# Performance work log

Hardware: AMD Instinct MI355X
Metric: run time of the kernel (lower is better)

Reference implementation:

```python
import jax, jax.numpy as jnp
import numpy as np
from jax import lax

V, E, H = 90000, 256, 512  # vocab, embed_dim, lstm_dim
B, TE, TD = 16, 64, 32     # batch, encoder time, decoder time
NEG = jnp.float32(-1e9)


def setup_inputs() -> dict:
    key = jax.random.key(0)
    ks = jax.random.split(key, 16)
    u = lambda k, shape, s: jax.random.uniform(k, shape, jnp.float32, -s, s)
    inp = {
        "encoder_inputs": jax.random.randint(ks[0], (B, TE), 0, V, dtype=jnp.int32),
        "decoder_inputs": jax.random.randint(ks[1], (B, TD), 0, V, dtype=jnp.int32),
        "encoder_lengths": jnp.maximum(jax.random.randint(ks[2], (B,), 1, TE + 1, dtype=jnp.int32), 1),
        "decoder_lengths": jnp.maximum(jax.random.randint(ks[3], (B,), 1, TD + 1, dtype=jnp.int32), 1),
        "embeddings": u(ks[4], (V, E), 1.0 / 16),
        # encoder BasicLSTMCell: kernel [E+H, 4H], bias [4H]
        "W_enc": u(ks[5], (E + H, 4 * H), 1.0 / np.sqrt(E + H)),
        "b_enc": jnp.zeros((4 * H,), jnp.float32),
        # decoder cell input = concat(embed, attention[H]) -> kernel [(E+H)+H, 4H]
        "W_dec": u(ks[6], (E + 2 * H, 4 * H), 1.0 / np.sqrt(E + 2 * H)),
        "b_dec": jnp.zeros((4 * H,), jnp.float32),
        # Bahdanau attention: memory layer, query layer, score vector v
        "W_mem": u(ks[7], (H, H), 1.0 / np.sqrt(H)),
        "W_query": u(ks[8], (H, H), 1.0 / np.sqrt(H)),
        "v_att": u(ks[9], (H,), 1.0 / np.sqrt(H)),
        # attention_layer: Dense(H, use_bias=False) on concat(cell_out, context)
        "W_attn": u(ks[10], (2 * H, H), 1.0 / np.sqrt(2 * H)),
        # output projection: Dense(90000, use_bias=False)
        "W_proj": u(ks[11], (H, V), 1.0 / np.sqrt(H)),
    }
    return inp


def _lstm_step(x, h, c, W, b):
    # TF BasicLSTMCell: gates i, j, f, o; forget_bias = 1.0
    z = jnp.concatenate([x, h], axis=-1) @ W + b
    i, j, f, o = jnp.split(z, 4, axis=-1)
    c2 = c * jax.nn.sigmoid(f + 1.0) + jax.nn.sigmoid(i) * jnp.tanh(j)
    h2 = jnp.tanh(c2) * jax.nn.sigmoid(o)
    return h2, c2


def reference(encoder_inputs, decoder_inputs, encoder_lengths, decoder_lengths,
              embeddings, W_enc, b_enc, W_dec, b_dec,
              W_mem, W_query, v_att, W_attn, W_proj):
    q_emb = embeddings[encoder_inputs]  # [B,TE,E]
    r_emb = embeddings[decoder_inputs]  # [B,TD,E]
    zeros_h = jnp.zeros((B, H), jnp.float32)

    # ---- encoder: dynamic_rnn semantics (zero outputs / frozen state past length)
    def enc_step(carry, xs):
        c, h = carry
        x_t, t = xs
        h2, c2 = _lstm_step(x_t, h, c, W_enc, b_enc)
        valid = (t < encoder_lengths)[:, None]
        h2 = jnp.where(valid, h2, h)
        c2 = jnp.where(valid, c2, c)
        return (c2, h2), jnp.where(valid, h2, 0.0)

    (c_e, h_e), enc_out = lax.scan(
        enc_step, (zeros_h, zeros_h),
        (q_emb.transpose(1, 0, 2), jnp.arange(TE)))
    enc_out = enc_out.transpose(1, 0, 2)  # [B,TE,H]

    keys = jnp.einsum('bth,hk->btk', enc_out, W_mem)  # memory layer
    enc_mask = jnp.arange(TE)[None, :] < encoder_lengths[:, None]  # [B,TE]

    # ---- decoder: AttentionWrapper(LSTM) + Bahdanau attention, per step
    def dec_step(carry, xs):
        c, h, attn = carry
        x_t, t = xs
        h2, c2 = _lstm_step(jnp.concatenate([x_t, attn], axis=-1), h, c, W_dec, b_dec)
        pq = h2 @ W_query  # [B,H]
        score = jnp.einsum('h,bth->bt', v_att, jnp.tanh(keys + pq[:, None, :]))
        score = jnp.where(enc_mask, score, NEG)
        align = jax.nn.softmax(score, axis=-1)
        ctx = jnp.einsum('bt,bth->bh', align, enc_out)
        attn2 = jnp.concatenate([h2, ctx], axis=-1) @ W_attn  # attention_layer
        logits_t = attn2 @ W_proj  # [B,V]
        # dynamic_decode zeros emissions once finished (t >= decoder_length)
        logits_t = jnp.where((t < decoder_lengths)[:, None], logits_t, 0.0)
        return (c2, h2, attn2), logits_t

    # initial state: zero_state cloned with cell_state = encoder final state
    _, logits = lax.scan(
        dec_step, (c_e, h_e, zeros_h),
        (r_emb.transpose(1, 0, 2), jnp.arange(TD)))
    return logits.transpose(1, 0, 2)  # [B,TD,V]
```

## Files before the change

kernel.cpp:

```cpp
#include <hip/hip_runtime.h>

#define E_  256
#define H_  512
#define B_  16
#define TE_ 64
#define TD_ 32
#define V_  90000
#define G4_ 2048
#define NBLK_ 128

typedef __attribute__((ext_vector_type(8))) short short8;
typedef __attribute__((ext_vector_type(4))) float f32x4;
typedef _Float16 half2_ __attribute__((ext_vector_type(2)));

__device__ __forceinline__ float sigm(float x) { return 1.f / (1.f + __expf(-x)); }
__device__ __forceinline__ float tanh_(float x) {
  float e = __expf(-2.f * fabsf(x));
  float r = (1.f - e) / (1.f + e);
  return x >= 0.f ? r : -r;
}
__device__ __forceinline__ unsigned short f2bf(float v) {
  union { float f; unsigned u; } c; c.f = v;
  unsigned r = c.u + 0x7FFFu + ((c.u >> 16) & 1u);
  return (unsigned short)(r >> 16);
}
__device__ __forceinline__ unsigned pack2(float a, float b) {
  union { unsigned u; _Float16 h[2]; } p;
  p.h[0] = (_Float16)a; p.h[1] = (_Float16)b;
  return p.u;
}
__device__ __forceinline__ float dot2u(unsigned w, unsigned h, float acc) {
#if __has_builtin(__builtin_amdgcn_fdot2)
  union { unsigned u; half2_ v; } a, b; a.u = w; b.u = h;
  return __builtin_amdgcn_fdot2(a.v, b.v, acc, false);
#else
  union { unsigned u; _Float16 h[2]; } a, b; a.u = w; b.u = h;
  return acc + (float)a.h[0] * (float)b.h[0] + (float)a.h[1] * (float)b.h[1];
#endif
}
__device__ __forceinline__ float dot8(uint4 w, uint4 h, float acc) {
  acc = dot2u(w.x, h.x, acc);
  acc = dot2u(w.y, h.y, acc);
  acc = dot2u(w.z, h.z, acc);
  acc = dot2u(w.w, h.w, acc);
  return acc;
}

__global__ __launch_bounds__(256) void k_cv(
    const float* __restrict__ W_enc, const float* __restrict__ W_dec,
    const float* __restrict__ W_query, const float* __restrict__ W_attn,
    const float* __restrict__ W_mem,
    uint4* __restrict__ Ue, uint4* __restrict__ Ud, uint4* __restrict__ Wq,
    uint4* __restrict__ Wa, uint4* __restrict__ Wm)
{
  int u = blockIdx.x * 256 + threadIdx.x;
  const float* src; uint4* dst; int C, r0, lu;
  if (u < 131072)      { src = W_enc;   dst = Ue; C = 2048; r0 = 256; lu = u; }
  else if (u < 393216) { src = W_dec;   dst = Ud; C = 2048; r0 = 256; lu = u - 131072; }
  else if (u < 425984) { src = W_query; dst = Wq; C = 512;  r0 = 0;   lu = u - 393216; }
  else if (u < 491520) { src = W_attn;  dst = Wa; C = 512;  r0 = 0;   lu = u - 425984; }
  else                 { src = W_mem;   dst = Wm; C = 512;  r0 = 0;   lu = u - 491520; }
  int kc = lu / C, col = lu - kc * C;
  union { uint4 v; _Float16 h[8]; } p;
  #pragma unroll
  for (int e = 0; e < 8; ++e)
    p.h[e] = (_Float16)src[(size_t)(r0 + kc * 8 + e) * C + col];
  dst[(size_t)kc * C + col] = p.v;
}

__global__ __launch_bounds__(256) void k_xg(
    const int* __restrict__ toks, const float* __restrict__ emb,
    const float* __restrict__ W, const float* __restrict__ bias,
    float* __restrict__ Xg)
{
  const int tid = threadIdx.x;
  const int cc = tid & 63;
  const int tg = tid >> 6;
  const int col = blockIdx.x * 64 + cc;
  const int t0 = blockIdx.y * 64 + tg * 16;
  const float* ep[16];
  #pragma unroll
  for (int i = 0; i < 16; ++i) ep[i] = emb + (size_t)toks[t0 + i] * E_;
  float acc[16];
  float bv = bias[col];
  #pragma unroll
  for (int i = 0; i < 16; ++i) acc[i] = bv;
  for (int k4 = 0; k4 < 64; ++k4) {
    float w0 = W[(size_t)(k4 * 4 + 0) * G4_ + col];
    float w1 = W[(size_t)(k4 * 4 + 1) * G4_ + col];
    float w2 = W[(size_t)(k4 * 4 + 2) * G4_ + col];
    float w3 = W[(size_t)(k4 * 4 + 3) * G4_ + col];
    #pragma unroll
    for (int i = 0; i < 16; ++i) {
      float4 e4 = *(const float4*)(ep[i] + k4 * 4);
      acc[i] += e4.x * w0 + e4.y * w1 + e4.z * w2 + e4.w * w3;
    }
  }
  #pragma unroll
  for (int i = 0; i < 16; ++i)
    Xg[(size_t)(t0 + i) * G4_ + col] = acc[i];
}

__device__ __forceinline__ void gbar(unsigned* bar, unsigned gen) {
  __syncthreads();
  if (threadIdx.x == 0) {
    __threadfence();
    __hip_atomic_fetch_add(bar, 1u, __ATOMIC_RELAXED, __HIP_MEMORY_SCOPE_AGENT);
    const unsigned tgt = gen * (unsigned)NBLK_;
    while (__hip_atomic_load(bar, __ATOMIC_RELAXED, __HIP_MEMORY_SCOPE_AGENT) < tgt)
      __builtin_amdgcn_s_sleep(1);
    __threadfence();
  }
  __syncthreads();
}

__global__ __launch_bounds__(512) void k_seq(
    const int* __restrict__ enc_len, const float* __restrict__ v_att,
    const float* __restrict__ Xge, const float* __restrict__ Xgd,
    const uint4* __restrict__ Ue, const uint4* __restrict__ Ud,
    const uint4* __restrict__ WqG, const uint4* __restrict__ WaG,
    const uint4* __restrict__ WmG,
    float* __restrict__ keys, unsigned* __restrict__ enc_f16,
    unsigned* __restrict__ hbuf, unsigned* __restrict__ abuf,
    unsigned short* __restrict__ attn_bf, unsigned* __restrict__ bar)
{
  __shared__ __align__(16) uint4 sU[128 * 16];
  __shared__ __align__(16) uint4 sE[64 * 16];
  __shared__ __align__(16) uint4 sI[128 * 16];
  __shared__ __align__(16) uint4 hbB[128];
  __shared__ float pacc[256];
  __shared__ float shx[4][16];
  __shared__ float shy[4][16];
  __shared__ float pqL[512];
  __shared__ float vlL[512];
  __shared__ float atf[512];
  __shared__ float scp[64][8];
  __shared__ float al64[64];
  __shared__ float ctp[256][2];

  const int tid = threadIdx.x, bid = blockIdx.x;
  const int tlo = tid & 255, hi = tid >> 8;
  const int b = tlo & 15, g = (tlo >> 4) & 3, hcl = tlo >> 6;
  const int wl = hcl * 4 + g;
  const int el = enc_len[b];
  const int elB = (bid < 16) ? enc_len[bid] : 0;
  unsigned gen = 0;

  for (int idx = tid; idx < 64 * 16; idx += 512) {
    int kc = idx >> 4, w = idx & 15;
    sE[idx] = Ue[(size_t)kc * 2048 + (w & 3) * 512 + bid * 4 + (w >> 2)];
  }
  for (int idx = tid; idx < 128 * 16; idx += 512) {
    int kc = idx >> 4, w = idx & 15;
    sU[idx] = Ud[(size_t)kc * 2048 + (w & 3) * 512 + bid * 4 + (w >> 2)];
  }
  if (tid < 32) abuf[bid * 32 + tid] = 0u;
  if (bid < 16) vlL[tid] = v_att[tid];

  float c = 0.f, hreg = 0.f;
  const uint4* hb4 = (const uint4*)hbuf;
  const uint4* ab4 = (const uint4*)abuf;
  const uint4* ef4 = (const uint4*)enc_f16;

  for (int t = 0; t < TE_; ++t) {
    for (int idx = tid; idx < 64 * 16; idx += 512) {
      int kc = idx >> 4, bb = idx & 15;
      uint4 v = {0u, 0u, 0u, 0u};
      if (t) v = hb4[bb * 64 + kc];
      sI[idx] = v;
    }
    __syncthreads();
    float acc;
    {
      const int kc0 = hi ? 32 : 0;
      acc = hi ? 0.f
               : Xge[(size_t)(b * TE_ + t) * G4_ + g * 512 + bid * 4 + hcl];
      const uint4* wp = sE + kc0 * 16 + wl;
      const uint4* ip = sI + kc0 * 16 + b;
      #pragma unroll 4
      for (int kc = 0; kc < 32; ++kc)
        acc = dot8(wp[kc * 16], ip[kc * 16], acc);
    }
    if (hi) pacc[tlo] = acc;
    __syncthreads();
    if (!hi) {
      acc += pacc[tlo];
      float v0 = acc;
      float v1 = __shfl_xor(v0, 16);
      float v2 = __shfl_xor(v0, 32);
      float v3 = __shfl_xor(v0, 48);
      float gi = (g == 0) ? v0 : (g == 1) ? v1 : (g == 2) ? v2 : v3;
      float gj = (g == 0) ? v1 : (g == 1) ? v0 : (g == 2) ? v3 : v2;
      float gf = (g == 0) ? v2 : (g == 1) ? v3 : (g == 2) ? v0 : v1;
      float go = (g == 0) ? v3 : (g == 1) ? v2 : (g == 2) ? v1 : v0;
      float c2 = c * sigm(gf + 1.f) + sigm(gi) * tanh_(gj);
      float h2 = tanh_(c2) * sigm(go);
      bool valid = t < el;
      c = valid ? c2 : c;
      hreg = valid ? h2 : hreg;
      if (g == 0) {
        shx[hcl][b] = hreg;
        shy[hcl][b] = valid ? h2 : 0.f;
      }
    }
    __syncthreads();
    if (tid < 32) {
      int bb = tid & 15, pr = tid >> 4;
      hbuf[bb * 256 + bid * 2 + pr] = pack2(shx[2 * pr][bb], shx[2 * pr + 1][bb]);
      enc_f16[(size_t)(bb * TE_ + t) * 256 + bid * 2 + pr] =
          pack2(shy[2 * pr][bb], shy[2 * pr + 1][bb]);
    }
    ++gen; gbar(bar, gen);
  }

  {
    for (int idx = tid; idx < 8 * 64; idx += 512) {
      int r = idx >> 6, kc = idx & 63;
      sI[idx] = ef4[(size_t)(bid * 8 + r) * 64 + kc];
    }
    __syncthreads();
    float a8[8] = {0.f, 0.f, 0.f, 0.f, 0.f, 0.f, 0.f, 0.f};
    const uint4* wm = WmG + tid;
    for (int kc = 0; kc < 64; ++kc) {
      uint4 w = wm[(size_t)kc * 512];
      #pragma unroll
      for (int r = 0; r < 8; ++r) a8[r] = dot8(w, sI[r * 64 + kc], a8[r]);
    }
    #pragma unroll
    for (int r = 0; r < 8; ++r)
      keys[(size_t)(bid * 8 + r) * 512 + tid] = a8[r];
    ++gen; gbar(bar, gen);
  }

  for (int t = 0; t < TD_; ++t) {
    for (int idx = tid; idx < 128 * 16; idx += 512) {
      int kc = idx >> 4, bb = idx & 15;
      sI[idx] = (kc < 64) ? ab4[bb * 64 + kc] : hb4[bb * 64 + (kc - 64)];
    }
    __syncthreads();
    float acc;
    {
      const int kc0 = hi ? 64 : 0;
      acc = hi ? 0.f
               : Xgd[(size_t)(b * TD_ + t) * G4_ + g * 512 + bid * 4 + hcl];
      const uint4* wp = sU + kc0 * 16 + wl;
      const uint4* ip = sI + kc0 * 16 + b;
      #pragma unroll 4
      for (int kc = 0; kc < 64; ++kc)
        acc = dot8(wp[kc * 16], ip[kc * 16], acc);
    }
    if (hi) pacc[tlo] = acc;
    __syncthreads();
    if (!hi) {
      acc += pacc[tlo];
      float v0 = acc;
      float v1 = __shfl_xor(v0, 16);
      float v2 = __shfl_xor(v0, 32);
      float v3 = __shfl_xor(v0, 48);
      float gi = (g == 0) ? v0 : (g == 1) ? v1 : (g == 2) ? v2 : v3;
      float gj = (g == 0) ? v1 : (g == 1) ? v0 : (g == 2) ? v3 : v2;
      float gf = (g == 0) ? v2 : (g == 1) ? v3 : (g == 2) ? v0 : v1;
      float go = (g == 0) ? v3 : (g == 1) ? v2 : (g == 2) ? v1 : v0;
      float c2 = c * sigm(gf + 1.f) + sigm(gi) * tanh_(gj);
      float h2 = tanh_(c2) * sigm(go);
      c = c2;
      if (g == 0) shx[hcl][b] = h2;
    }
    __syncthreads();
    if (tid < 32) {
      int bb = tid & 15, pr = tid >> 4;
      hbuf[bb * 256 + bid * 2 + pr] = pack2(shx[2 * pr][bb], shx[2 * pr + 1][bb]);
    }
    ++gen; gbar(bar, gen);

    if (bid < 16) {
      if (tid < 64) hbB[tid] = hb4[bid * 64 + tid];
      __syncthreads();
      {
        float a = 0.f;
        const uint4* wq = WqG + tid;
        #pragma unroll 4
        for (int kc = 0; kc < 64; ++kc)
          a = dot8(wq[(size_t)kc * 512], hbB[kc], a);
        pqL[tid] = a;
      }
      __syncthreads();
      {
        int tt = tid >> 3, q = tid & 7;
        const float4* kr = (const float4*)(keys + (size_t)(bid * TE_ + tt) * 512 + q * 64);
        const float4* pp = (const float4*)(pqL + q * 64);
        const float4* vp = (const float4*)(vlL + q * 64);
        float s = 0.f;
        #pragma unroll 4
        for (int i = 0; i < 16; ++i) {
          float4 k4 = kr[i], p4 = pp[i], v4 = vp[i];
          s += v4.x * tanh_(k4.x + p4.x) + v4.y * tanh_(k4.y + p4.y)
             + v4.z * tanh_(k4.z + p4.z) + v4.w * tanh_(k4.w + p4.w);
        }
        scp[tt][q] = s;
      }
      __syncthreads();
      if (tid < 64) {
        float sum = 0.f;
        #pragma unroll
        for (int q = 0; q < 8; ++q) sum += scp[tid][q];
        float sc = (tid < elB) ? sum : -1e9f;
        float m = sc;
        for (int o = 32; o > 0; o >>= 1) m = fmaxf(m, __shfl_xor(m, o));
        float p = __expf(sc - m);
        float l = p;
        for (int o = 32; o > 0; o >>= 1) l += __shfl_xor(l, o);
        al64[tid] = p / l;
      }
      __syncthreads();
      {
        const int j = tlo;
        float c0 = 0.f, c1 = 0.f;
        const unsigned* eb = enc_f16 + (size_t)(bid * TE_ + hi * 32) * 256 + j;
        #pragma unroll 8
        for (int t2 = 0; t2 < 32; ++t2) {
          union { unsigned u; _Float16 h[2]; } u2;
          u2.u = eb[(size_t)t2 * 256];
          float a = al64[hi * 32 + t2];
          c0 += a * (float)u2.h[0];
          c1 += a * (float)u2.h[1];
        }
        if (hi) { ctp[j][0] = c0; ctp[j][1] = c1; }
        __syncthreads();
        if (!hi)
          ((unsigned*)hbB)[256 + j] = pack2(c0 + ctp[j][0], c1 + ctp[j][1]);
        __syncthreads();
      }
      {
        float a = 0.f;
        const uint4* wa = WaG + tid;
        #pragma unroll 2
        for (int kc = 0; kc < 128; ++kc)
          a = dot8(wa[(size_t)kc * 512], hbB[kc], a);
        attn_bf[(size_t)(bid * TD_ + t) * 512 + tid] = f2bf(a);
        atf[tid] = a;
      }
      __syncthreads();
      if (tid < 256) abuf[bid * 256 + tid] = pack2(atf[2 * tid], atf[2 * tid + 1]);
    }
    ++gen; gbar(bar, gen);
  }
}

__global__ __launch_bounds__(512) void k_proj(
    const float* __restrict__ Wp, const unsigned short* __restrict__ Abf,
    const int* __restrict__ dec_len_g, float* __restrict__ out)
{
  __shared__ unsigned short Al[512 * 40];
  __shared__ unsigned short Bl[128 * 40];
  __shared__ int dl[16];
  const int tid = threadIdx.x;
  const int n0 = blockIdx.x * 128;
  const int wave = tid >> 6, lane = tid & 63;
  if (tid < 16) dl[tid] = dec_len_g[tid];
  f32x4 acc[4][8] = {};
  for (int kc = 0; kc < 16; ++kc) {
    const int k0 = kc * 32;
    {
      const unsigned short* src = Abf + (size_t)tid * 512 + k0;
      unsigned short* dst = Al + tid * 40;
      *(uint4*)(dst)      = *(const uint4*)(src);
      *(uint4*)(dst + 8)  = *(const uint4*)(src + 8);
      *(uint4*)(dst + 16) = *(const uint4*)(src + 16);
      *(uint4*)(dst + 24) = *(const uint4*)(src + 24);
    }
    {
      int kk = tid >> 4;
      int nn = (tid & 15) * 8;
      const float* src = Wp + (size_t)(k0 + kk) * V_ + n0 + nn;
      #pragma unroll
      for (int j = 0; j < 8; ++j) {
        float v = (n0 + nn + j < V_) ? src[j] : 0.f;
        Bl[(nn + j) * 40 + kk] = f2bf(v);
      }
    }
    __syncthreads();
    short8 bfr[8];
    #pragma unroll
    for (int nt = 0; nt < 8; ++nt)
      bfr[nt] = *(const short8*)&Bl[(nt * 16 + (lane & 15)) * 40 + (lane >> 4) * 8];
    #pragma unroll
    for (int mt = 0; mt < 4; ++mt) {
      short8 af = *(const short8*)&Al[(wave * 64 + mt * 16 + (lane & 15)) * 40 + (lane >> 4) * 8];
      #pragma unroll
      for (int nt = 0; nt < 8; ++nt)
        acc[mt][nt] = __builtin_amdgcn_mfma_f32_16x16x32_bf16(af, bfr[nt], acc[mt][nt], 0, 0, 0);
    }
    __syncthreads();
  }
  #pragma unroll
  for (int mt = 0; mt < 4; ++mt) {
    #pragma unroll
    for (int e = 0; e < 4; ++e) {
      int r = wave * 64 + mt * 16 + ((lane >> 4) << 2) + e;
      bool valid = (r & 31) < dl[r >> 5];
      #pragma unroll
      for (int nt = 0; nt < 8; ++nt) {
        int gcol = n0 + nt * 16 + (lane & 15);
        if (gcol < V_)
          out[(size_t)r * V_ + gcol] = valid ? acc[mt][nt][e] : 0.f;
      }
    }
  }
}

extern "C" void kernel_launch(void* const* d_in, const int* in_sizes, int n_in,
                              void* d_out, int out_size, void* d_ws, size_t ws_size,
                              hipStream_t stream) {
  const int* enc_in   = (const int*)d_in[0];
  const int* dec_in   = (const int*)d_in[1];
  const int* enc_len  = (const int*)d_in[2];
  const int* dec_len  = (const int*)d_in[3];
  const float* emb    = (const float*)d_in[4];
  const float* W_enc  = (const float*)d_in[5];
  const float* b_enc  = (const float*)d_in[6];
  const float* W_dec  = (const float*)d_in[7];
  const float* b_dec  = (const float*)d_in[8];
  const float* W_mem  = (const float*)d_in[9];
  const float* W_query= (const float*)d_in[10];
  const float* v_att  = (const float*)d_in[11];
  const float* W_attn = (const float*)d_in[12];
  const float* W_proj = (const float*)d_in[13];
  float* out = (float*)d_out;
  char* ws = (char*)d_ws;

  float* Xge          = (float*)(ws + 0);
  float* Xgd          = (float*)(ws + 8388608);
  uint4* Ue           = (uint4*)(ws + 12582912);
  uint4* Ud           = (uint4*)(ws + 14680064);
  uint4* Wq           = (uint4*)(ws + 18874368);
  uint4* Wa           = (uint4*)(ws + 19398656);
  uint4* Wm           = (uint4*)(ws + 20447232);
  unsigned* hbuf      = (unsigned*)(ws + 20971520);
  unsigned* abuf      = (unsigned*)(ws + 20987904);
  unsigned* bar       = (unsigned*)(ws + 21004288);
  unsigned* enc_f16   = (unsigned*)(ws + 23068672);
  float* keys         = (float*)(ws + 24117248);
  unsigned short* attn_bf = (unsigned short*)(ws + 26214400);

  k_cv<<<2048, 256, 0, stream>>>(W_enc, W_dec, W_query, W_attn, W_mem,
                                 Ue, Ud, Wq, Wa, Wm);
  k_xg<<<dim3(32, 16), 256, 0, stream>>>(enc_in, emb, W_enc, b_enc, Xge);
  k_xg<<<dim3(32, 8),  256, 0, stream>>>(dec_in, emb, W_dec, b_dec, Xgd);
  hipMemsetAsync(bar, 0, 64, stream);
  {
    const int* a0 = enc_len; const float* a1 = v_att;
    const float* a2 = Xge;   const float* a3 = Xgd;
    const uint4* a4 = Ue;    const uint4* a5 = Ud;
    const uint4* a6 = Wq;    const uint4* a7 = Wa;
    const uint4* a8 = Wm;
    float* a9 = keys;        unsigned* a10 = enc_f16;
    unsigned* a11 = hbuf;    unsigned* a12 = abuf;
    unsigned short* a13 = attn_bf; unsigned* a14 = bar;
    void* kargs[] = { &a0, &a1, &a2, &a3, &a4, &a5, &a6, &a7, &a8,
                      &a9, &a10, &a11, &a12, &a13, &a14 };
    hipLaunchCooperativeKernel((void*)k_seq, dim3(NBLK_), dim3(512),
                               kargs, 0, stream);
  }
  k_proj<<<704, 512, 0, stream>>>(W_proj, attn_bf, dec_len, out);
}
```

Measured before the change: 2.676 ms.

## Use lightweight grid barriers with agent-scope atomics and double-buffered hidden state

Replaces the __threadfence-based grid barrier with a lite version that only waits on outstanding memory counters, and routes cross-block hidden/attention state through agent-scope relaxed atomic loads and stores. The hidden-state buffer is double-buffered so each step reads the previous step's buffer while writing a new one, which removes write-after-read hazards once the fences are gone. Heavy barriers are kept where ordinary stores (enc_f16, keys) must become visible. This aims to cut per-step barrier latency in the persistent recurrent kernel, at the cost of scalar 4-byte loads instead of uint4 loads and reliance on subtle memory-ordering assumptions.

```diff
diff --git a/kernel.cpp b/kernel.cpp
--- a/kernel.cpp
+++ b/kernel.cpp
@@ -44,6 +44,13 @@
   acc = dot2u(w.z, h.z, acc);
   acc = dot2u(w.w, h.w, acc);
   return acc;
+}
+
+__device__ __forceinline__ unsigned ld_ag(const unsigned* p) {
+  return __hip_atomic_load(p, __ATOMIC_RELAXED, __HIP_MEMORY_SCOPE_AGENT);
+}
+__device__ __forceinline__ void st_ag(unsigned* p, unsigned v) {
+  __hip_atomic_store(p, v, __ATOMIC_RELAXED, __HIP_MEMORY_SCOPE_AGENT);
 }
 
 __global__ __launch_bounds__(256) void k_cv(
@@ -101,7 +108,18 @@
     Xg[(size_t)(t0 + i) * G4_ + col] = acc[i];
 }
 
-__device__ __forceinline__ void gbar(unsigned* bar, unsigned gen) {
+__device__ __forceinline__ void gbar_lite(unsigned* bar, unsigned gen) {
+  __syncthreads();
+  if (threadIdx.x == 0) {
+    asm volatile("s_waitcnt vmcnt(0) lgkmcnt(0)" ::: "memory");
+    __hip_atomic_fetch_add(bar, 1u, __ATOMIC_RELAXED, __HIP_MEMORY_SCOPE_AGENT);
+    const unsigned tgt = gen * (unsigned)NBLK_;
+    while (__hip_atomic_load(bar, __ATOMIC_RELAXED, __HIP_MEMORY_SCOPE_AGENT) < tgt)
+      __builtin_amdgcn_s_sleep(1);
+  }
+  __syncthreads();
+}
+__device__ __forceinline__ void gbar_heavy(unsigned* bar, unsigned gen) {
   __syncthreads();
   if (threadIdx.x == 0) {
     __threadfence();
@@ -127,7 +145,7 @@
   __shared__ __align__(16) uint4 sU[128 * 16];
   __shared__ __align__(16) uint4 sE[64 * 16];
   __shared__ __align__(16) uint4 sI[128 * 16];
-  __shared__ __align__(16) uint4 hbB[128];
+  __shared__ __align__(16) unsigned sHC[512];
   __shared__ float pacc[256];
   __shared__ float shx[4][16];
   __shared__ float shy[4][16];
@@ -145,6 +163,9 @@
   const int el = enc_len[b];
   const int elB = (bid < 16) ? enc_len[bid] : 0;
   unsigned gen = 0;
+  unsigned* const hb0 = hbuf;
+  unsigned* const hb1 = hbuf + 4096;
+  unsigned* sIu = (unsigned*)sI;
 
   for (int idx = tid; idx < 64 * 16; idx += 512) {
     int kc = idx >> 4, w = idx & 15;
@@ -154,20 +175,22 @@
     int kc = idx >> 4, w = idx & 15;
     sU[idx] = Ud[(size_t)kc * 2048 + (w & 3) * 512 + bid * 4 + (w >> 2)];
   }
-  if (tid < 32) abuf[bid * 32 + tid] = 0u;
+  if (tid < 32) st_ag(abuf + bid * 32 + tid, 0u);
   if (bid < 16) vlL[tid] = v_att[tid];
 
   float c = 0.f, hreg = 0.f;
-  const uint4* hb4 = (const uint4*)hbuf;
-  const uint4* ab4 = (const uint4*)abuf;
   const uint4* ef4 = (const uint4*)enc_f16;
 
   for (int t = 0; t < TE_; ++t) {
-    for (int idx = tid; idx < 64 * 16; idx += 512) {
-      int kc = idx >> 4, bb = idx & 15;
-      uint4 v = {0u, 0u, 0u, 0u};
-      if (t) v = hb4[bb * 64 + kc];
-      sI[idx] = v;
+    unsigned* hb_prev = (t & 1) ? hb0 : hb1;
+    unsigned* hb_cur  = (t & 1) ? hb1 : hb0;
+    if (t == 0) {
+      for (int idx = tid; idx < 4096; idx += 512) sIu[idx] = 0u;
+    } else {
+      for (int idx = tid; idx < 4096; idx += 512) {
+        int w = idx & 3, bb = (idx >> 2) & 15, kc = idx >> 6;
+        sIu[idx] = ld_ag(hb_prev + bb * 256 + kc * 4 + w);
+      }
     }
     __syncthreads();
     float acc;
@@ -206,11 +229,13 @@
     __syncthreads();
     if (tid < 32) {
       int bb = tid & 15, pr = tid >> 4;
-      hbuf[bb * 256 + bid * 2 + pr] = pack2(shx[2 * pr][bb], shx[2 * pr + 1][bb]);
+      st_ag(hb_cur + bb * 256 + bid * 2 + pr, pack2(shx[2 * pr][bb], shx[2 * pr + 1][bb]));
       enc_f16[(size_t)(bb * TE_ + t) * 256 + bid * 2 + pr] =
           pack2(shy[2 * pr][bb], shy[2 * pr + 1][bb]);
     }
-    ++gen; gbar(bar, gen);
+    ++gen;
+    if (t == TE_ - 1) gbar_heavy(bar, gen);
+    else              gbar_lite(bar, gen);
   }
 
   {
@@ -229,13 +254,16 @@
     #pragma unroll
     for (int r = 0; r < 8; ++r)
       keys[(size_t)(bid * 8 + r) * 512 + tid] = a8[r];
-    ++gen; gbar(bar, gen);
+    ++gen; gbar_heavy(bar, gen);
   }
 
   for (int t = 0; t < TD_; ++t) {
-    for (int idx = tid; idx < 128 * 16; idx += 512) {
-      int kc = idx >> 4, bb = idx & 15;
-      sI[idx] = (kc < 64) ? ab4[bb * 64 + kc] : hb4[bb * 64 + (kc - 64)];
+    unsigned* hb_prev = (t & 1) ? hb0 : hb1;
+    unsigned* hb_cur  = (t & 1) ? hb1 : hb0;
+    for (int idx = tid; idx < 8192; idx += 512) {
+      int w = idx & 3, bb = (idx >> 2) & 15, kc = idx >> 6;
+      sIu[idx] = (kc < 64) ? ld_ag(abuf + bb * 256 + kc * 4 + w)
+                           : ld_ag(hb_prev + bb * 256 + (kc - 64) * 4 + w);
     }
     __syncthreads();
     float acc;
@@ -269,19 +297,20 @@
     __syncthreads();
     if (tid < 32) {
       int bb = tid & 15, pr = tid >> 4;
-      hbuf[bb * 256 + bid * 2 + pr] = pack2(shx[2 * pr][bb], shx[2 * pr + 1][bb]);
-    }
-    ++gen; gbar(bar, gen);
+      st_ag(hb_cur + bb * 256 + bid * 2 + pr, pack2(shx[2 * pr][bb], shx[2 * pr + 1][bb]));
+    }
+    ++gen; gbar_lite(bar, gen);
 
     if (bid < 16) {
-      if (tid < 64) hbB[tid] = hb4[bid * 64 + tid];
+      if (tid < 256) sHC[tid] = ld_ag(hb_cur + bid * 256 + tid);
       __syncthreads();
       {
         float a = 0.f;
+        const uint4* hv = (const uint4*)sHC;
         const uint4* wq = WqG + tid;
         #pragma unroll 4
         for (int kc = 0; kc < 64; ++kc)
-          a = dot8(wq[(size_t)kc * 512], hbB[kc], a);
+          a = dot8(wq[(size_t)kc * 512], hv[kc], a);
         pqL[tid] = a;
       }
       __syncthreads();
@@ -328,22 +357,23 @@
         if (hi) { ctp[j][0] = c0; ctp[j][1] = c1; }
         __syncthreads();
         if (!hi)
-          ((unsigned*)hbB)[256 + j] = pack2(c0 + ctp[j][0], c1 + ctp[j][1]);
+          sHC[256 + j] = pack2(c0 + ctp[j][0], c1 + ctp[j][1]);
         __syncthreads();
       }
       {
         float a = 0.f;
+        const uint4* iv2 = (const uint4*)sHC;
         const uint4* wa = WaG + tid;
         #pragma unroll 2
         for (int kc = 0; kc < 128; ++kc)
-          a = dot8(wa[(size_t)kc * 512], hbB[kc], a);
+          a = dot8(wa[(size_t)kc * 512], iv2[kc], a);
         attn_bf[(size_t)(bid * TD_ + t) * 512 + tid] = f2bf(a);
         atf[tid] = a;
       }
       __syncthreads();
-      if (tid < 256) abuf[bid * 256 + tid] = pack2(atf[2 * tid], atf[2 * tid + 1]);
-    }
-    ++gen; gbar(bar, gen);
+      if (tid < 256) st_ag(abuf + bid * 256 + tid, pack2(atf[2 * tid], atf[2 * tid + 1]));
+    }
+    ++gen; gbar_lite(bar, gen);
   }
 }
 
@@ -437,8 +467,8 @@
   uint4* Wa           = (uint4*)(ws + 19398656);
   uint4* Wm           = (uint4*)(ws + 20447232);
   unsigned* hbuf      = (unsigned*)(ws + 20971520);
-  unsigned* abuf      = (unsigned*)(ws + 20987904);
-  unsigned* bar       = (unsigned*)(ws + 21004288);
+  unsigned* abuf      = (unsigned*)(ws + 21004288);
+  unsigned* bar       = (unsigned*)(ws + 21020672);
   unsigned* enc_f16   = (unsigned*)(ws + 23068672);
   float* keys         = (float*)(ws + 24117248);
   unsigned short* attn_bf = (unsigned short*)(ws + 26214400);
```

New measurement: 2.186 ms. 1.22x faster.
